# Optimization experiments

Hardware: AMD Instinct MI355X
Metric: run time of the kernel (lower is better)

The kernel has to match this reference:

```python
import jax, jax.numpy as jnp
import numpy as np

N_LAYERS = 2
D_MODEL = 1024
EXPAND = 2
D_INNER = EXPAND * D_MODEL   # 2048
D_STATE = 16
D_CONV = 4
DT_RANK = (D_MODEL + 15) // 16  # 64
BATCH = 2
SEQ = 1024


def setup_inputs() -> dict:
    key = jax.random.key(0)
    ks = jax.random.split(key, 8)
    x = jax.random.normal(ks[0], (BATCH, SEQ, D_MODEL), jnp.float32)
    in_proj_w = jax.random.normal(ks[1], (N_LAYERS, 2 * D_INNER, D_MODEL), jnp.float32) * 0.02
    conv_w = jax.random.normal(ks[2], (N_LAYERS, D_INNER, 1, D_CONV), jnp.float32) * 0.2
    conv_b = jnp.zeros((N_LAYERS, D_INNER), jnp.float32)
    x_proj_w = jax.random.normal(ks[3], (N_LAYERS, DT_RANK + 2 * D_STATE, D_INNER), jnp.float32) * 0.02
    dt_proj_w = jax.random.normal(ks[4], (N_LAYERS, D_INNER, DT_RANK), jnp.float32) * 0.1
    # softplus(b) ~ 0.01 -> realistic small dt init
    dt_proj_b = jnp.full((N_LAYERS, D_INNER), float(np.log(np.expm1(0.01))), jnp.float32)
    A_log = jnp.tile(jnp.log(jnp.arange(1, D_STATE + 1, dtype=jnp.float32))[None, None, :], (N_LAYERS, D_INNER, 1))
    D = jnp.ones((N_LAYERS, D_INNER), jnp.float32)
    out_proj_w = jax.random.normal(ks[5], (N_LAYERS, D_MODEL, D_INNER), jnp.float32) * 0.02
    return {
        'x': x, 'in_proj_w': in_proj_w, 'conv_w': conv_w, 'conv_b': conv_b,
        'x_proj_w': x_proj_w, 'dt_proj_w': dt_proj_w, 'dt_proj_b': dt_proj_b,
        'A_log': A_log, 'D': D, 'out_proj_w': out_proj_w,
    }


def _mamba_block(x, W_in, w_c, b_c, W_x, W_dt, b_dt, A_log, Dp, W_out):
    # x: (B, L, d_model)
    xz = jnp.einsum('bld,ed->ble', x, W_in)           # (B, L, 2*d_inner)
    xc, z = jnp.split(xz, 2, axis=-1)
    # causal depthwise conv1d over time
    xc = xc.transpose(0, 2, 1)                         # (B, d_inner, L)
    xc = jax.lax.conv_general_dilated(
        xc, w_c, window_strides=(1,), padding=[(D_CONV - 1, 0)],
        dimension_numbers=('NCH', 'OIH', 'NCH'), feature_group_count=D_INNER,
    ) + b_c[None, :, None]
    u = jax.nn.silu(xc).transpose(0, 2, 1)             # (B, L, d_inner)
    # input-dependent dt, B, C
    x_dbl = jnp.einsum('bld,ed->ble', u, W_x)          # (B, L, dt_rank+2N)
    dt, Bm, Cm = jnp.split(x_dbl, [DT_RANK, DT_RANK + D_STATE], axis=-1)
    delta = jax.nn.softplus(jnp.einsum('blr,dr->bld', dt, W_dt) + b_dt)  # (B, L, d_inner)
    A = -jnp.exp(A_log)                                 # (d_inner, N)
    dA = jnp.exp(jnp.einsum('bld,dn->bldn', delta, A))  # (B, L, d_inner, N)
    dBu = jnp.einsum('bld,bln,bld->bldn', delta, Bm, u) # (B, L, d_inner, N)

    def step(h, inp):
        dA_t, dBu_t, C_t = inp                          # (B,d,N), (B,d,N), (B,N)
        h = dA_t * h + dBu_t
        return h, jnp.einsum('bdn,bn->bd', h, C_t)

    h0 = jnp.zeros((x.shape[0], D_INNER, D_STATE), x.dtype)
    _, ys = jax.lax.scan(step, h0, (dA.transpose(1, 0, 2, 3), dBu.transpose(1, 0, 2, 3), Cm.transpose(1, 0, 2)))
    y = ys.transpose(1, 0, 2) + u * Dp                  # (B, L, d_inner)
    y = y * jax.nn.silu(z)
    return jnp.einsum('bld,od->blo', y, W_out)          # (B, L, d_model)


def _forward(x, in_proj_w, conv_w, conv_b, x_proj_w, dt_proj_w, dt_proj_b, A_log, D, out_proj_w):
    residual = x
    for i in range(N_LAYERS):
        x = _mamba_block(x, in_proj_w[i], conv_w[i], conv_b[i], x_proj_w[i],
                         dt_proj_w[i], dt_proj_b[i], A_log[i], D[i], out_proj_w[i])
    return x + residual


def reference(x, in_proj_w, conv_w, conv_b, x_proj_w, dt_proj_w, dt_proj_b, A_log, D, out_proj_w):
    return _forward(x, in_proj_w, conv_w, conv_b, x_proj_w, dt_proj_w, dt_proj_b, A_log, D, out_proj_w)
```

## Files before the change

kernel.cpp:

```cpp
#include <hip/hip_runtime.h>
#include <hip/hip_bf16.h>

#define NLAYERS 2
#define DMODEL 1024
#define DINNER 2048
#define DSTATE 16
#define DCONV 4
#define DTRANK 64
#define BATCH 2
#define SEQ 1024
#define TOK (BATCH * SEQ)

#define NCHUNK 32
#define CLEN (SEQ / NCHUNK)
#define KSX 16
#define KSO 4

typedef short bf16x8 __attribute__((ext_vector_type(8)));
typedef float f32x4 __attribute__((ext_vector_type(4)));
typedef unsigned short ushort8 __attribute__((ext_vector_type(8)));

__device__ __forceinline__ float softplusf(float x) {
    return (x > 20.f) ? x : log1pf(__expf(x));
}
__device__ __forceinline__ float siluf(float x) {
    return x / (1.f + __expf(-x));
}
__device__ __forceinline__ unsigned short f2bf(float f) {
    union { float f; unsigned int u; } v; v.f = f;
    const unsigned int r = (v.u + 0x7FFFu + ((v.u >> 16) & 1u)) >> 16;
    return (unsigned short)r;
}
__device__ __forceinline__ float bf2f(unsigned short s) {
    union { unsigned int u; float f; } v; v.u = ((unsigned int)s) << 16;
    return v.f;
}

__device__ __forceinline__ int swz_granule(int row, int kq) {
    return (row >> 1) * 8 + ((((row & 1) << 2) | kq) ^ ((row >> 1) & 7));
}

__device__ __forceinline__ void cvt8(const float* __restrict__ in,
                                     unsigned short* __restrict__ out, int i) {
    const float4 a = reinterpret_cast<const float4*>(in)[i * 2 + 0];
    const float4 b = reinterpret_cast<const float4*>(in)[i * 2 + 1];
    ushort4 o0, o1;
    o0.x = f2bf(a.x); o0.y = f2bf(a.y); o0.z = f2bf(a.z); o0.w = f2bf(a.w);
    o1.x = f2bf(b.x); o1.y = f2bf(b.y); o1.z = f2bf(b.z); o1.w = f2bf(b.w);
    reinterpret_cast<ushort4*>(out)[i * 2 + 0] = o0;
    reinterpret_cast<ushort4*>(out)[i * 2 + 1] = o1;
}

#define WI8 1048576
#define WO8 524288
#define WX8 49152
#define WD8 32768
#define AC8 262144
__global__ __launch_bounds__(256)
void cvt_all(const float* __restrict__ wi, const float* __restrict__ wo,
             const float* __restrict__ wx, const float* __restrict__ wd,
             const float* __restrict__ xin,
             unsigned short* __restrict__ wi_bf, unsigned short* __restrict__ wo_bf,
             unsigned short* __restrict__ wx_bf, unsigned short* __restrict__ wd_bf,
             unsigned short* __restrict__ act_bf) {
    int i = blockIdx.x * 256 + threadIdx.x;
    if (i < WI8) { cvt8(wi, wi_bf, i); return; }
    i -= WI8;
    if (i < WO8) { cvt8(wo, wo_bf, i); return; }
    i -= WO8;
    if (i < WX8) { cvt8(wx, wx_bf, i); return; }
    i -= WX8;
    if (i < WD8) { cvt8(wd, wd_bf, i); return; }
    i -= WD8;
    if (i < AC8) { cvt8(xin, act_bf, i); return; }
}

template <int EPI>
__global__ __launch_bounds__(256)
void gemm_bf16(const unsigned short* __restrict__ Ab, int lda,
               const unsigned short* __restrict__ Wb, int ldw,
               void* __restrict__ Cptr, int ldc, int kLen, int Nw,
               size_t cSlice, const float* __restrict__ bias) {
    __shared__ unsigned short As[2][128 * 32];
    __shared__ unsigned short Bs[2][128 * 32];
    const int tid = threadIdx.x;
    const int wave = tid >> 6, lane = tid & 63;
    const int wr = wave >> 1, wc = wave & 1;
    const int m0 = blockIdx.y * 128, n0 = blockIdx.x * 128;
    const int kbeg = blockIdx.z * kLen;
    const int r = lane & 15, kq = lane >> 4;
    const int nt = kLen >> 5;

    const int ch0 = tid, ch1 = 256 + tid;
    const int g0 = ch0 >> 3, p0 = ch0 & 7, lp0 = p0 ^ (g0 & 7);
    const int srow0 = (g0 << 1) | (lp0 >> 2), skq0 = lp0 & 3;
    const int g1 = ch1 >> 3, p1 = ch1 & 7, lp1 = p1 ^ (g1 & 7);
    const int srow1 = (g1 << 1) | (lp1 >> 2), skq1 = lp1 & 3;
    const int wrow0 = min(n0 + srow0, Nw - 1);
    const int wrow1 = min(n0 + srow1, Nw - 1);

    auto stage = [&](int buf, int kt) {
        __builtin_amdgcn_global_load_lds(
            (const __attribute__((address_space(1))) void*)
                &Ab[(size_t)(m0 + srow0) * lda + kt + skq0 * 8],
            (__attribute__((address_space(3))) void*)&As[buf][ch0 * 8], 16, 0, 0);
        __builtin_amdgcn_global_load_lds(
            (const __attribute__((address_space(1))) void*)
                &Wb[(size_t)wrow0 * ldw + kt + skq0 * 8],
            (__attribute__((address_space(3))) void*)&Bs[buf][ch0 * 8], 16, 0, 0);
        __builtin_amdgcn_global_load_lds(
            (const __attribute__((address_space(1))) void*)
                &Ab[(size_t)(m0 + srow1) * lda + kt + skq1 * 8],
            (__attribute__((address_space(3))) void*)&As[buf][ch1 * 8], 16, 0, 0);
        __builtin_amdgcn_global_load_lds(
            (const __attribute__((address_space(1))) void*)
                &Wb[(size_t)wrow1 * ldw + kt + skq1 * 8],
            (__attribute__((address_space(3))) void*)&Bs[buf][ch1 * 8], 16, 0, 0);
    };

    int aoff[4], boff[4];
#pragma unroll
    for (int f = 0; f < 4; ++f) {
        aoff[f] = swz_granule(wr * 64 + f * 16 + r, kq) * 8;
        boff[f] = swz_granule(wc * 64 + f * 16 + r, kq) * 8;
    }

    f32x4 acc[4][4] = {};
    stage(0, kbeg);
    for (int t = 0; t < nt; ++t) {
        const int cur = t & 1;
        if (t + 1 < nt) {
            stage(cur ^ 1, kbeg + (t + 1) * 32);
            asm volatile("s_waitcnt vmcnt(4)" ::: "memory");
        } else {
            asm volatile("s_waitcnt vmcnt(0)" ::: "memory");
        }
        __builtin_amdgcn_s_barrier();
        __builtin_amdgcn_sched_barrier(0);
        bf16x8 a[4], b[4];
#pragma unroll
        for (int f = 0; f < 4; ++f) {
            a[f] = *reinterpret_cast<const bf16x8*>(&As[cur][aoff[f]]);
            b[f] = *reinterpret_cast<const bf16x8*>(&Bs[cur][boff[f]]);
        }
#pragma unroll
        for (int fi = 0; fi < 4; ++fi)
#pragma unroll
            for (int fj = 0; fj < 4; ++fj)
                acc[fi][fj] = __builtin_amdgcn_mfma_f32_16x16x32_bf16(
                    a[fi], b[fj], acc[fi][fj], 0, 0, 0);
        __builtin_amdgcn_sched_barrier(0);
        asm volatile("s_waitcnt lgkmcnt(0)" ::: "memory");
        __builtin_amdgcn_s_barrier();
    }

    const int cr = lane >> 4, cc = lane & 15;
#pragma unroll
    for (int fi = 0; fi < 4; ++fi)
#pragma unroll
        for (int fj = 0; fj < 4; ++fj)
#pragma unroll
            for (int p = 0; p < 4; ++p) {
                const int m = m0 + wr * 64 + fi * 16 + cr * 4 + p;
                const int n = n0 + wc * 64 + fj * 16 + cc;
                const float v = acc[fi][fj][p];
                if (EPI == 0) {
                    if (n < Nw)
                        ((float*)Cptr)[(size_t)blockIdx.z * cSlice +
                                       (size_t)m * ldc + n] = v;
                } else if (EPI == 3) {
                    ((unsigned short*)Cptr)[(size_t)blockIdx.z * cSlice +
                                            (size_t)m * ldc + n] = f2bf(v);
                } else if (EPI == 4) {
                    ((unsigned short*)Cptr)[(size_t)m * ldc + n] =
                        f2bf(softplusf(v + bias[n]));
                } else {
                    if (n < Nw)
                        ((unsigned short*)Cptr)[(size_t)blockIdx.z * cSlice +
                                                (size_t)m * ldc + n] = f2bf(v);
                }
            }
}

__global__ __launch_bounds__(256)
void conv_silu8(const unsigned short* __restrict__ xz_bf,
                const float* __restrict__ cw,
                const float* __restrict__ cb,
                unsigned short* __restrict__ u_bf) {
    const int gid = blockIdx.x * 256 + threadIdx.x;
    const int d8 = gid & 255;
    const int t = gid >> 8;
    const int l = t & (SEQ - 1);
    const int d0 = d8 * 8;

    float cwv[8][4];
#pragma unroll
    for (int j = 0; j < 8; ++j) {
        const float4 c = *reinterpret_cast<const float4*>(&cw[(d0 + j) * DCONV]);
        cwv[j][0] = c.x; cwv[j][1] = c.y; cwv[j][2] = c.z; cwv[j][3] = c.w;
    }
    float acc[8];
    {
        const float4 b0 = *reinterpret_cast<const float4*>(&cb[d0]);
        const float4 b1 = *reinterpret_cast<const float4*>(&cb[d0 + 4]);
        acc[0] = b0.x; acc[1] = b0.y; acc[2] = b0.z; acc[3] = b0.w;
        acc[4] = b1.x; acc[5] = b1.y; acc[6] = b1.z; acc[7] = b1.w;
    }
#pragma unroll
    for (int k = 0; k < DCONV; ++k) {
        const int li = l - (DCONV - 1) + k;
        if (li >= 0) {
            const ushort8 v = *reinterpret_cast<const ushort8*>(
                &xz_bf[(size_t)(t - (DCONV - 1) + k) * 4096 + d0]);
#pragma unroll
            for (int j = 0; j < 8; ++j)
                acc[j] = fmaf(cwv[j][k], bf2f(v[j]), acc[j]);
        }
    }
    ushort8 o;
#pragma unroll
    for (int j = 0; j < 8; ++j) o[j] = f2bf(siluf(acc[j]));
    *reinterpret_cast<ushort8*>(&u_bf[(size_t)t * DINNER + d0]) = o;
}

__global__ __launch_bounds__(256)
void reduce_x(const unsigned short* __restrict__ part, float* __restrict__ xdbl,
              unsigned short* __restrict__ dt_bf) {
    const int i = blockIdx.x * 256 + threadIdx.x;
    if (i >= TOK * 96) return;
    float s = 0.f;
#pragma unroll
    for (int k = 0; k < KSX; ++k) s += bf2f(part[(size_t)k * (TOK * 96) + i]);
    xdbl[i] = s;
    const int t = i / 96, c = i - t * 96;
    if (c < DTRANK) dt_bf[t * DTRANK + c] = f2bf(s);
}

template <int MODE>
__global__ __launch_bounds__(256)
void reduce_out(const unsigned short* __restrict__ part,
                const float* __restrict__ resid, void* __restrict__ outp) {
    const int i = blockIdx.x * 256 + threadIdx.x;
    if (i >= TOK * DMODEL / 4) return;
    float s[4] = {0.f, 0.f, 0.f, 0.f};
#pragma unroll
    for (int k = 0; k < KSO; ++k) {
        const ushort4 p = reinterpret_cast<const ushort4*>(
            &part[(size_t)k * (TOK * DMODEL)])[i];
        s[0] += bf2f(p.x); s[1] += bf2f(p.y); s[2] += bf2f(p.z); s[3] += bf2f(p.w);
    }
    if (MODE == 0) {
        ushort4 o;
        o.x = f2bf(s[0]); o.y = f2bf(s[1]); o.z = f2bf(s[2]); o.w = f2bf(s[3]);
        reinterpret_cast<ushort4*>(outp)[i] = o;
    } else {
        const float4 rr = reinterpret_cast<const float4*>(resid)[i];
        float4 o;
        o.x = s[0] + rr.x; o.y = s[1] + rr.y; o.z = s[2] + rr.z; o.w = s[3] + rr.w;
        reinterpret_cast<float4*>(outp)[i] = o;
    }
}

__device__ __forceinline__ void load_b16(const float* __restrict__ p, float* B) {
    const float4* bp = reinterpret_cast<const float4*>(p);
    const float4 b0 = bp[0], b1 = bp[1], b2 = bp[2], b3 = bp[3];
    B[0] = b0.x; B[1] = b0.y; B[2] = b0.z; B[3] = b0.w;
    B[4] = b1.x; B[5] = b1.y; B[6] = b1.z; B[7] = b1.w;
    B[8] = b2.x; B[9] = b2.y; B[10] = b2.z; B[11] = b2.w;
    B[12] = b3.x; B[13] = b3.y; B[14] = b3.z; B[15] = b3.w;
}
__device__ __forceinline__ void load_bf16x16(const unsigned short* __restrict__ p,
                                             float* B) {
    const ushort8 v0 = *reinterpret_cast<const ushort8*>(p);
    const ushort8 v1 = *reinterpret_cast<const ushort8*>(p + 8);
#pragma unroll
    for (int j = 0; j < 8; ++j) { B[j] = bf2f(v0[j]); B[8 + j] = bf2f(v1[j]); }
}
__device__ __forceinline__ void store_bf16x16(unsigned short* __restrict__ p,
                                              const float* B) {
    ushort8 v0, v1;
#pragma unroll
    for (int j = 0; j < 8; ++j) { v0[j] = f2bf(B[j]); v1[j] = f2bf(B[8 + j]); }
    *reinterpret_cast<ushort8*>(p) = v0;
    *reinterpret_cast<ushort8*>(p + 8) = v1;
}

__global__ __launch_bounds__(256)
void scan_partial(const unsigned short* __restrict__ delta_bf,
                  const unsigned short* __restrict__ u_bf,
                  const float* __restrict__ xdbl,
                  const float* __restrict__ A_log,
                  unsigned short* __restrict__ hbuf,
                  unsigned short* __restrict__ Pbuf) {
    const int b = blockIdx.y / NCHUNK;
    const int c = blockIdx.y % NCHUNK;
    const int d = blockIdx.x * 256 + threadIdx.x;
    const int t0 = b * SEQ + c * CLEN;

    float A_dn[16];
    load_b16(&A_log[d * DSTATE], A_dn);
#pragma unroll
    for (int n = 0; n < 16; ++n) A_dn[n] = -__expf(A_dn[n]);

    float h[16];
#pragma unroll
    for (int n = 0; n < 16; ++n) h[n] = 0.f;
    float sdlt = 0.f;

    float dltA, uvA, BA[16];
    float dltB, uvB, BB[16];
    dltA = bf2f(delta_bf[(size_t)t0 * DINNER + d]);
    uvA = bf2f(u_bf[(size_t)t0 * DINNER + d]);
    load_b16(&xdbl[(size_t)t0 * 96 + DTRANK], BA);

#define PSTEP(dlt_, uv_, Bc_)                              \
    {                                                      \
        const float du = (dlt_) * (uv_);                   \
        sdlt += (dlt_);                                    \
        _Pragma("unroll")                                  \
        for (int n = 0; n < 16; ++n) {                     \
            const float dA = __expf((dlt_) * A_dn[n]);     \
            h[n] = fmaf(dA, h[n], du * Bc_[n]);            \
        }                                                  \
    }

    for (int l = 0; l < CLEN; l += 2) {
        const int t = t0 + l;
        dltB = bf2f(delta_bf[(size_t)(t + 1) * DINNER + d]);
        uvB = bf2f(u_bf[(size_t)(t + 1) * DINNER + d]);
        load_b16(&xdbl[(size_t)(t + 1) * 96 + DTRANK], BB);
        PSTEP(dltA, uvA, BA);
        if (l + 2 < CLEN) {
            dltA = bf2f(delta_bf[(size_t)(t + 2) * DINNER + d]);
            uvA = bf2f(u_bf[(size_t)(t + 2) * DINNER + d]);
            load_b16(&xdbl[(size_t)(t + 2) * 96 + DTRANK], BA);
        }
        PSTEP(dltB, uvB, BB);
    }
#undef PSTEP

    float P[16];
#pragma unroll
    for (int n = 0; n < 16; ++n) P[n] = __expf(sdlt * A_dn[n]);

    const size_t base = ((size_t)(b * NCHUNK + c) * DINNER + d) * DSTATE;
    store_bf16x16(&hbuf[base], h);
    store_bf16x16(&Pbuf[base], P);
}

__global__ __launch_bounds__(256)
void scan_combine(unsigned short* __restrict__ hbuf,
                  const unsigned short* __restrict__ Pbuf) {
    const int gid = blockIdx.x * 256 + threadIdx.x;
    const int b = gid / (DINNER * DSTATE);
    const int dn = gid - b * (DINNER * DSTATE);
    const size_t base = (size_t)b * NCHUNK * DINNER * DSTATE + dn;
    float hv[NCHUNK], Pv[NCHUNK];
#pragma unroll
    for (int c = 0; c < NCHUNK; ++c) {
        const size_t idx = base + (size_t)c * (DINNER * DSTATE);
        hv[c] = bf2f(hbuf[idx]);
        Pv[c] = bf2f(Pbuf[idx]);
    }
    float hi = 0.f;
#pragma unroll
    for (int c = 0; c < NCHUNK; ++c) {
        const size_t idx = base + (size_t)c * (DINNER * DSTATE);
        hbuf[idx] = f2bf(hi);
        hi = fmaf(Pv[c], hi, hv[c]);
    }
}

__global__ __launch_bounds__(256)
void scan_final(const unsigned short* __restrict__ delta_bf,
                const unsigned short* __restrict__ u_bf,
                const float* __restrict__ xdbl,
                const unsigned short* __restrict__ xz_bf,
                const float* __restrict__ A_log,
                const float* __restrict__ Dp,
                const unsigned short* __restrict__ hbuf,
                unsigned short* __restrict__ yout) {
    const int b = blockIdx.y / NCHUNK;
    const int c = blockIdx.y % NCHUNK;
    const int d = blockIdx.x * 256 + threadIdx.x;
    const int t0 = b * SEQ + c * CLEN;

    float A_dn[16];
    load_b16(&A_log[d * DSTATE], A_dn);
#pragma unroll
    for (int n = 0; n < 16; ++n) A_dn[n] = -__expf(A_dn[n]);
    const float Dd = Dp[d];

    float h[16];
    load_bf16x16(&hbuf[((size_t)(b * NCHUNK + c) * DINNER + d) * DSTATE], h);

    float dltA, uvA, BA[16], CA[16];
    float dltB, uvB, BB[16], CB[16];
    dltA = bf2f(delta_bf[(size_t)t0 * DINNER + d]);
    uvA = bf2f(u_bf[(size_t)t0 * DINNER + d]);
    load_b16(&xdbl[(size_t)t0 * 96 + DTRANK], BA);
    load_b16(&xdbl[(size_t)t0 * 96 + DTRANK + DSTATE], CA);

#define FSTEP(t_, dlt_, uv_, Bc_, Cc_)                          \
    {                                                           \
        const float du = (dlt_) * (uv_);                        \
        _Pragma("unroll")                                       \
        for (int n = 0; n < 16; ++n) {                          \
            const float dA = __expf((dlt_) * A_dn[n]);          \
            h[n] = fmaf(dA, h[n], du * Bc_[n]);                 \
        }                                                       \
        float s0 = 0.f, s1 = 0.f, s2 = 0.f, s3 = 0.f;           \
        _Pragma("unroll")                                       \
        for (int q = 0; q < 4; ++q) {                           \
            s0 = fmaf(h[q*4+0], Cc_[q*4+0], s0);                \
            s1 = fmaf(h[q*4+1], Cc_[q*4+1], s1);                \
            s2 = fmaf(h[q*4+2], Cc_[q*4+2], s2);                \
            s3 = fmaf(h[q*4+3], Cc_[q*4+3], s3);                \
        }                                                       \
        const float zv = bf2f(xz_bf[(size_t)(t_) * 4096 + 2048 + d]); \
        const float y = (s0 + s1) + (s2 + s3) + (uv_) * Dd;     \
        yout[(size_t)(t_) * DINNER + d] = f2bf(y * siluf(zv));  \
    }

    for (int l = 0; l < CLEN; l += 2) {
        const int t = t0 + l;
        dltB = bf2f(delta_bf[(size_t)(t + 1) * DINNER + d]);
        uvB = bf2f(u_bf[(size_t)(t + 1) * DINNER + d]);
        load_b16(&xdbl[(size_t)(t + 1) * 96 + DTRANK], BB);
        load_b16(&xdbl[(size_t)(t + 1) * 96 + DTRANK + DSTATE], CB);
        FSTEP(t, dltA, uvA, BA, CA);
        if (l + 2 < CLEN) {
            dltA = bf2f(delta_bf[(size_t)(t + 2) * DINNER + d]);
            uvA = bf2f(u_bf[(size_t)(t + 2) * DINNER + d]);
            load_b16(&xdbl[(size_t)(t + 2) * 96 + DTRANK], BA);
            load_b16(&xdbl[(size_t)(t + 2) * 96 + DTRANK + DSTATE], CA);
        }
        FSTEP(t + 1, dltB, uvB, BB, CB);
    }
#undef FSTEP
}

extern "C" void kernel_launch(void* const* d_in, const int* in_sizes, int n_in,
                              void* d_out, int out_size, void* d_ws, size_t ws_size,
                              hipStream_t stream) {
    const float* x          = (const float*)d_in[0];
    const float* in_proj_w  = (const float*)d_in[1];
    const float* conv_w     = (const float*)d_in[2];
    const float* conv_b     = (const float*)d_in[3];
    const float* x_proj_w   = (const float*)d_in[4];
    const float* dt_proj_w  = (const float*)d_in[5];
    const float* dt_proj_b  = (const float*)d_in[6];
    const float* A_log      = (const float*)d_in[7];
    const float* Dp         = (const float*)d_in[8];
    const float* out_proj_w = (const float*)d_in[9];
    float* out = (float*)d_out;

    float* ws = (float*)d_ws;
    float* xdbl  = ws;
    unsigned short* us = (unsigned short*)(xdbl + 196608);
    unsigned short* xpart  = us;
    unsigned short* hbuf   = xpart + 3145728;
    unsigned short* Pbuf   = hbuf + 2097152;
    unsigned short* opart  = Pbuf + 2097152;
    unsigned short* wi_bf  = opart + 8388608;
    unsigned short* wo_bf  = wi_bf + 8388608;
    unsigned short* wx_bf  = wo_bf + 4194304;
    unsigned short* wd_bf  = wx_bf + 393216;
    unsigned short* xz_bf  = wd_bf + 262144;
    unsigned short* u_bf   = xz_bf + 8388608;
    unsigned short* dlt_bf = u_bf  + 4194304;
    unsigned short* act_bf = dlt_bf + 4194304;
    unsigned short* y_bf   = act_bf + 2097152;
    unsigned short* dt_bf  = y_bf  + 4194304;

    cvt_all<<<(WI8 + WO8 + WX8 + WD8 + AC8 + 255) / 256, 256, 0, stream>>>(
        in_proj_w, out_proj_w, x_proj_w, dt_proj_w, x,
        wi_bf, wo_bf, wx_bf, wd_bf, act_bf);

    for (int layer = 0; layer < NLAYERS; ++layer) {
        const unsigned short* Wi = wi_bf + (size_t)layer * (2 * DINNER) * DMODEL;
        const unsigned short* Wo = wo_bf + (size_t)layer * DMODEL * DINNER;
        const unsigned short* Wx = wx_bf + (size_t)layer * 96 * DINNER;
        const unsigned short* Wd = wd_bf + (size_t)layer * DINNER * DTRANK;
        const float* cw = conv_w    + (size_t)layer * DINNER * DCONV;
        const float* cb = conv_b    + (size_t)layer * DINNER;
        const float* bd = dt_proj_b + (size_t)layer * DINNER;
        const float* Al = A_log     + (size_t)layer * DINNER * DSTATE;
        const float* Dl = Dp        + (size_t)layer * DINNER;

        {
            dim3 grid(4096 / 128, TOK / 128, 1);
            gemm_bf16<3><<<grid, 256, 0, stream>>>(act_bf, DMODEL, Wi, DMODEL,
                                                   xz_bf, 2 * DINNER, DMODEL,
                                                   2 * DINNER, 0, nullptr);
        }
        conv_silu8<<<(TOK * 256) / 256, 256, 0, stream>>>(xz_bf, cw, cb, u_bf);
        {
            dim3 grid(1, TOK / 128, KSX);
            gemm_bf16<5><<<grid, 256, 0, stream>>>(u_bf, DINNER, Wx, DINNER,
                                                   xpart, 96, DINNER / KSX, 96,
                                                   (size_t)TOK * 96, nullptr);
            reduce_x<<<(TOK * 96 + 255) / 256, 256, 0, stream>>>(xpart, xdbl, dt_bf);
        }
        {
            dim3 grid(DINNER / 128, TOK / 128, 1);
            gemm_bf16<4><<<grid, 256, 0, stream>>>(dt_bf, DTRANK, Wd, DTRANK,
                                                   dlt_bf, DINNER, DTRANK, DINNER,
                                                   0, bd);
        }
        {
            dim3 gridA(DINNER / 256, BATCH * NCHUNK);
            scan_partial<<<gridA, 256, 0, stream>>>(dlt_bf, u_bf, xdbl, Al,
                                                    hbuf, Pbuf);
            scan_combine<<<(BATCH * DINNER * DSTATE) / 256, 256, 0, stream>>>(hbuf, Pbuf);
            scan_final<<<gridA, 256, 0, stream>>>(dlt_bf, u_bf, xdbl, xz_bf,
                                                  Al, Dl, hbuf, y_bf);
        }
        {
            dim3 grid(DMODEL / 128, TOK / 128, KSO);
            gemm_bf16<3><<<grid, 256, 0, stream>>>(y_bf, DINNER, Wo, DINNER,
                                                   opart, DMODEL, DINNER / KSO,
                                                   DMODEL, (size_t)TOK * DMODEL,
                                                   nullptr);
            const int nred = TOK * DMODEL / 4;
            if (layer == NLAYERS - 1) {
                reduce_out<1><<<(nred + 255) / 256, 256, 0, stream>>>(opart, x, out);
            } else {
                reduce_out<0><<<(nred + 255) / 256, 256, 0, stream>>>(opart, nullptr,
                                                                      act_bf);
            }
        }
    }
}
```

Baseline: 320.5 us.

## Fold scan combine into final scan, pack B/C as bf16, remap GEMM tile order

Removes the scan_combine kernel: each scan_final block now recomputes its chunk-initial state by iterating over all preceding chunks' partial states and decay products, which adds redundant work that grows with the chunk index. B and C are stored as a compact bf16 array of 32 values per token instead of fp32 inside the 96-wide xdbl buffer, which halves the bytes read per step in the scans but loses precision on B and C. GEMM workgroup IDs are remapped in interleaved groups of eight, apparently to spread neighbouring tiles across XCDs or improve cache locality. The unused fp32 epilogue is dropped.

New measurement: 340.6 us. +6.3%, slower.

```diff
diff --git a/kernel.cpp b/kernel.cpp
--- a/kernel.cpp
+++ b/kernel.cpp
@@ -86,7 +86,14 @@
     const int tid = threadIdx.x;
     const int wave = tid >> 6, lane = tid & 63;
     const int wr = wave >> 1, wc = wave & 1;
-    const int m0 = blockIdx.y * 128, n0 = blockIdx.x * 128;
+
+    const int nwg = gridDim.x * gridDim.y;
+    const int id0 = blockIdx.y * gridDim.x + blockIdx.x;
+    const int cpx = nwg >> 3;
+    const int id = (id0 & 7) * cpx + (id0 >> 3);
+    const int bx = id % gridDim.x, by = id / gridDim.x;
+
+    const int m0 = by * 128, n0 = bx * 128;
     const int kbeg = blockIdx.z * kLen;
     const int r = lane & 15, kq = lane >> 4;
     const int nt = kLen >> 5;
@@ -164,11 +171,7 @@
                 const int m = m0 + wr * 64 + fi * 16 + cr * 4 + p;
                 const int n = n0 + wc * 64 + fj * 16 + cc;
                 const float v = acc[fi][fj][p];
-                if (EPI == 0) {
-                    if (n < Nw)
-                        ((float*)Cptr)[(size_t)blockIdx.z * cSlice +
-                                       (size_t)m * ldc + n] = v;
-                } else if (EPI == 3) {
+                if (EPI == 3) {
                     ((unsigned short*)Cptr)[(size_t)blockIdx.z * cSlice +
                                             (size_t)m * ldc + n] = f2bf(v);
                 } else if (EPI == 4) {
@@ -224,16 +227,17 @@
 }
 
 __global__ __launch_bounds__(256)
-void reduce_x(const unsigned short* __restrict__ part, float* __restrict__ xdbl,
+void reduce_x(const unsigned short* __restrict__ part,
+              unsigned short* __restrict__ bc_bf,
               unsigned short* __restrict__ dt_bf) {
     const int i = blockIdx.x * 256 + threadIdx.x;
     if (i >= TOK * 96) return;
     float s = 0.f;
 #pragma unroll
     for (int k = 0; k < KSX; ++k) s += bf2f(part[(size_t)k * (TOK * 96) + i]);
-    xdbl[i] = s;
     const int t = i / 96, c = i - t * 96;
     if (c < DTRANK) dt_bf[t * DTRANK + c] = f2bf(s);
+    else            bc_bf[t * 32 + (c - DTRANK)] = f2bf(s);
 }
 
 template <int MODE>
@@ -288,7 +292,7 @@
 __global__ __launch_bounds__(256)
 void scan_partial(const unsigned short* __restrict__ delta_bf,
                   const unsigned short* __restrict__ u_bf,
-                  const float* __restrict__ xdbl,
+                  const unsigned short* __restrict__ bc_bf,
                   const float* __restrict__ A_log,
                   unsigned short* __restrict__ hbuf,
                   unsigned short* __restrict__ Pbuf) {
@@ -311,7 +315,7 @@
     float dltB, uvB, BB[16];
     dltA = bf2f(delta_bf[(size_t)t0 * DINNER + d]);
     uvA = bf2f(u_bf[(size_t)t0 * DINNER + d]);
-    load_b16(&xdbl[(size_t)t0 * 96 + DTRANK], BA);
+    load_bf16x16(&bc_bf[(size_t)t0 * 32], BA);
 
 #define PSTEP(dlt_, uv_, Bc_)                              \
     {                                                      \
@@ -328,12 +332,12 @@
         const int t = t0 + l;
         dltB = bf2f(delta_bf[(size_t)(t + 1) * DINNER + d]);
         uvB = bf2f(u_bf[(size_t)(t + 1) * DINNER + d]);
-        load_b16(&xdbl[(size_t)(t + 1) * 96 + DTRANK], BB);
+        load_bf16x16(&bc_bf[(size_t)(t + 1) * 32], BB);
         PSTEP(dltA, uvA, BA);
         if (l + 2 < CLEN) {
             dltA = bf2f(delta_bf[(size_t)(t + 2) * DINNER + d]);
             uvA = bf2f(u_bf[(size_t)(t + 2) * DINNER + d]);
-            load_b16(&xdbl[(size_t)(t + 2) * 96 + DTRANK], BA);
+            load_bf16x16(&bc_bf[(size_t)(t + 2) * 32], BA);
         }
         PSTEP(dltB, uvB, BB);
     }
@@ -349,36 +353,14 @@
 }
 
 __global__ __launch_bounds__(256)
-void scan_combine(unsigned short* __restrict__ hbuf,
-                  const unsigned short* __restrict__ Pbuf) {
-    const int gid = blockIdx.x * 256 + threadIdx.x;
-    const int b = gid / (DINNER * DSTATE);
-    const int dn = gid - b * (DINNER * DSTATE);
-    const size_t base = (size_t)b * NCHUNK * DINNER * DSTATE + dn;
-    float hv[NCHUNK], Pv[NCHUNK];
-#pragma unroll
-    for (int c = 0; c < NCHUNK; ++c) {
-        const size_t idx = base + (size_t)c * (DINNER * DSTATE);
-        hv[c] = bf2f(hbuf[idx]);
-        Pv[c] = bf2f(Pbuf[idx]);
-    }
-    float hi = 0.f;
-#pragma unroll
-    for (int c = 0; c < NCHUNK; ++c) {
-        const size_t idx = base + (size_t)c * (DINNER * DSTATE);
-        hbuf[idx] = f2bf(hi);
-        hi = fmaf(Pv[c], hi, hv[c]);
-    }
-}
-
-__global__ __launch_bounds__(256)
 void scan_final(const unsigned short* __restrict__ delta_bf,
                 const unsigned short* __restrict__ u_bf,
-                const float* __restrict__ xdbl,
+                const unsigned short* __restrict__ bc_bf,
                 const unsigned short* __restrict__ xz_bf,
                 const float* __restrict__ A_log,
                 const float* __restrict__ Dp,
                 const unsigned short* __restrict__ hbuf,
+                const unsigned short* __restrict__ Pbuf,
                 unsigned short* __restrict__ yout) {
     const int b = blockIdx.y / NCHUNK;
     const int c = blockIdx.y % NCHUNK;
@@ -392,14 +374,23 @@
     const float Dd = Dp[d];
 
     float h[16];
-    load_bf16x16(&hbuf[((size_t)(b * NCHUNK + c) * DINNER + d) * DSTATE], h);
+#pragma unroll
+    for (int n = 0; n < 16; ++n) h[n] = 0.f;
+    for (int cc = 0; cc < c; ++cc) {
+        const size_t base = ((size_t)(b * NCHUNK + cc) * DINNER + d) * DSTATE;
+        float hl[16], Pc[16];
+        load_bf16x16(&hbuf[base], hl);
+        load_bf16x16(&Pbuf[base], Pc);
+#pragma unroll
+        for (int n = 0; n < 16; ++n) h[n] = fmaf(Pc[n], h[n], hl[n]);
+    }
 
     float dltA, uvA, BA[16], CA[16];
     float dltB, uvB, BB[16], CB[16];
     dltA = bf2f(delta_bf[(size_t)t0 * DINNER + d]);
     uvA = bf2f(u_bf[(size_t)t0 * DINNER + d]);
-    load_b16(&xdbl[(size_t)t0 * 96 + DTRANK], BA);
-    load_b16(&xdbl[(size_t)t0 * 96 + DTRANK + DSTATE], CA);
+    load_bf16x16(&bc_bf[(size_t)t0 * 32], BA);
+    load_bf16x16(&bc_bf[(size_t)t0 * 32 + 16], CA);
 
 #define FSTEP(t_, dlt_, uv_, Bc_, Cc_)                          \
     {                                                           \
@@ -426,14 +417,14 @@
         const int t = t0 + l;
         dltB = bf2f(delta_bf[(size_t)(t + 1) * DINNER + d]);
         uvB = bf2f(u_bf[(size_t)(t + 1) * DINNER + d]);
-        load_b16(&xdbl[(size_t)(t + 1) * 96 + DTRANK], BB);
-        load_b16(&xdbl[(size_t)(t + 1) * 96 + DTRANK + DSTATE], CB);
+        load_bf16x16(&bc_bf[(size_t)(t + 1) * 32], BB);
+        load_bf16x16(&bc_bf[(size_t)(t + 1) * 32 + 16], CB);
         FSTEP(t, dltA, uvA, BA, CA);
         if (l + 2 < CLEN) {
             dltA = bf2f(delta_bf[(size_t)(t + 2) * DINNER + d]);
             uvA = bf2f(u_bf[(size_t)(t + 2) * DINNER + d]);
-            load_b16(&xdbl[(size_t)(t + 2) * 96 + DTRANK], BA);
-            load_b16(&xdbl[(size_t)(t + 2) * 96 + DTRANK + DSTATE], CA);
+            load_bf16x16(&bc_bf[(size_t)(t + 2) * 32], BA);
+            load_bf16x16(&bc_bf[(size_t)(t + 2) * 32 + 16], CA);
         }
         FSTEP(t + 1, dltB, uvB, BB, CB);
     }
@@ -455,11 +446,10 @@
     const float* out_proj_w = (const float*)d_in[9];
     float* out = (float*)d_out;
 
-    float* ws = (float*)d_ws;
-    float* xdbl  = ws;
-    unsigned short* us = (unsigned short*)(xdbl + 196608);
+    unsigned short* us = (unsigned short*)d_ws;
     unsigned short* xpart  = us;
-    unsigned short* hbuf   = xpart + 3145728;
+    unsigned short* bc_bf  = xpart + 3145728;
+    unsigned short* hbuf   = bc_bf + 65536;
     unsigned short* Pbuf   = hbuf + 2097152;
     unsigned short* opart  = Pbuf + 2097152;
     unsigned short* wi_bf  = opart + 8388608;
@@ -500,7 +490,8 @@
             gemm_bf16<5><<<grid, 256, 0, stream>>>(u_bf, DINNER, Wx, DINNER,
                                                    xpart, 96, DINNER / KSX, 96,
                                                    (size_t)TOK * 96, nullptr);
-            reduce_x<<<(TOK * 96 + 255) / 256, 256, 0, stream>>>(xpart, xdbl, dt_bf);
+            reduce_x<<<(TOK * 96 + 255) / 256, 256, 0, stream>>>(xpart, bc_bf,
+                                                                 dt_bf);
         }
         {
             dim3 grid(DINNER / 128, TOK / 128, 1);
@@ -510,11 +501,10 @@
         }
         {
             dim3 gridA(DINNER / 256, BATCH * NCHUNK);
-            scan_partial<<<gridA, 256, 0, stream>>>(dlt_bf, u_bf, xdbl, Al,
+            scan_partial<<<gridA, 256, 0, stream>>>(dlt_bf, u_bf, bc_bf, Al,
                                                     hbuf, Pbuf);
-            scan_combine<<<(BATCH * DINNER * DSTATE) / 256, 256, 0, stream>>>(hbuf, Pbuf);
-            scan_final<<<gridA, 256, 0, stream>>>(dlt_bf, u_bf, xdbl, xz_bf,
-                                                  Al, Dl, hbuf, y_bf);
+            scan_final<<<gridA, 256, 0, stream>>>(dlt_bf, u_bf, bc_bf, xz_bf,
+                                                  Al, Dl, hbuf, Pbuf, y_bf);
         }
         {
             dim3 grid(DMODEL / 128, TOK / 128, KSO);
```

## Fuse chunked scan passes into one cooperative kernel with grid syncs

Applied to the files above, without the earlier changes.

Merges the three scan kernels (per-chunk partial scan, cross-chunk combine, final output scan) into one cooperative launch that separates the phases with grid-wide syncs. The aim is to remove two kernel launches and their launch gaps per layer. The grid is 8x64 = 512 blocks of 256 threads, and every block must be co-resident for the cooperative launch to work. Register pressure from holding the combine arrays may also lower occupancy. The now-unused EPI==0 GEMM epilogue is also removed.

Result: slower. 805.6 us (+151.4%).

```diff
diff --git a/kernel.cpp b/kernel.cpp
--- a/kernel.cpp
+++ b/kernel.cpp
@@ -1,5 +1,8 @@
 #include <hip/hip_runtime.h>
 #include <hip/hip_bf16.h>
+#include <hip/hip_cooperative_groups.h>
+
+namespace cg = cooperative_groups;
 
 #define NLAYERS 2
 #define DMODEL 1024
@@ -164,11 +167,7 @@
                 const int m = m0 + wr * 64 + fi * 16 + cr * 4 + p;
                 const int n = n0 + wc * 64 + fj * 16 + cc;
                 const float v = acc[fi][fj][p];
-                if (EPI == 0) {
-                    if (n < Nw)
-                        ((float*)Cptr)[(size_t)blockIdx.z * cSlice +
-                                       (size_t)m * ldc + n] = v;
-                } else if (EPI == 3) {
+                if (EPI == 3) {
                     ((unsigned short*)Cptr)[(size_t)blockIdx.z * cSlice +
                                             (size_t)m * ldc + n] = f2bf(v);
                 } else if (EPI == 4) {
@@ -286,100 +285,16 @@
 }
 
 __global__ __launch_bounds__(256)
-void scan_partial(const unsigned short* __restrict__ delta_bf,
-                  const unsigned short* __restrict__ u_bf,
-                  const float* __restrict__ xdbl,
-                  const float* __restrict__ A_log,
-                  unsigned short* __restrict__ hbuf,
-                  unsigned short* __restrict__ Pbuf) {
-    const int b = blockIdx.y / NCHUNK;
-    const int c = blockIdx.y % NCHUNK;
-    const int d = blockIdx.x * 256 + threadIdx.x;
-    const int t0 = b * SEQ + c * CLEN;
-
-    float A_dn[16];
-    load_b16(&A_log[d * DSTATE], A_dn);
-#pragma unroll
-    for (int n = 0; n < 16; ++n) A_dn[n] = -__expf(A_dn[n]);
-
-    float h[16];
-#pragma unroll
-    for (int n = 0; n < 16; ++n) h[n] = 0.f;
-    float sdlt = 0.f;
-
-    float dltA, uvA, BA[16];
-    float dltB, uvB, BB[16];
-    dltA = bf2f(delta_bf[(size_t)t0 * DINNER + d]);
-    uvA = bf2f(u_bf[(size_t)t0 * DINNER + d]);
-    load_b16(&xdbl[(size_t)t0 * 96 + DTRANK], BA);
-
-#define PSTEP(dlt_, uv_, Bc_)                              \
-    {                                                      \
-        const float du = (dlt_) * (uv_);                   \
-        sdlt += (dlt_);                                    \
-        _Pragma("unroll")                                  \
-        for (int n = 0; n < 16; ++n) {                     \
-            const float dA = __expf((dlt_) * A_dn[n]);     \
-            h[n] = fmaf(dA, h[n], du * Bc_[n]);            \
-        }                                                  \
-    }
-
-    for (int l = 0; l < CLEN; l += 2) {
-        const int t = t0 + l;
-        dltB = bf2f(delta_bf[(size_t)(t + 1) * DINNER + d]);
-        uvB = bf2f(u_bf[(size_t)(t + 1) * DINNER + d]);
-        load_b16(&xdbl[(size_t)(t + 1) * 96 + DTRANK], BB);
-        PSTEP(dltA, uvA, BA);
-        if (l + 2 < CLEN) {
-            dltA = bf2f(delta_bf[(size_t)(t + 2) * DINNER + d]);
-            uvA = bf2f(u_bf[(size_t)(t + 2) * DINNER + d]);
-            load_b16(&xdbl[(size_t)(t + 2) * 96 + DTRANK], BA);
-        }
-        PSTEP(dltB, uvB, BB);
-    }
-#undef PSTEP
-
-    float P[16];
-#pragma unroll
-    for (int n = 0; n < 16; ++n) P[n] = __expf(sdlt * A_dn[n]);
-
-    const size_t base = ((size_t)(b * NCHUNK + c) * DINNER + d) * DSTATE;
-    store_bf16x16(&hbuf[base], h);
-    store_bf16x16(&Pbuf[base], P);
-}
-
-__global__ __launch_bounds__(256)
-void scan_combine(unsigned short* __restrict__ hbuf,
-                  const unsigned short* __restrict__ Pbuf) {
-    const int gid = blockIdx.x * 256 + threadIdx.x;
-    const int b = gid / (DINNER * DSTATE);
-    const int dn = gid - b * (DINNER * DSTATE);
-    const size_t base = (size_t)b * NCHUNK * DINNER * DSTATE + dn;
-    float hv[NCHUNK], Pv[NCHUNK];
-#pragma unroll
-    for (int c = 0; c < NCHUNK; ++c) {
-        const size_t idx = base + (size_t)c * (DINNER * DSTATE);
-        hv[c] = bf2f(hbuf[idx]);
-        Pv[c] = bf2f(Pbuf[idx]);
-    }
-    float hi = 0.f;
-#pragma unroll
-    for (int c = 0; c < NCHUNK; ++c) {
-        const size_t idx = base + (size_t)c * (DINNER * DSTATE);
-        hbuf[idx] = f2bf(hi);
-        hi = fmaf(Pv[c], hi, hv[c]);
-    }
-}
-
-__global__ __launch_bounds__(256)
-void scan_final(const unsigned short* __restrict__ delta_bf,
+void scan_fused(const unsigned short* __restrict__ delta_bf,
                 const unsigned short* __restrict__ u_bf,
                 const float* __restrict__ xdbl,
                 const unsigned short* __restrict__ xz_bf,
                 const float* __restrict__ A_log,
                 const float* __restrict__ Dp,
-                const unsigned short* __restrict__ hbuf,
+                unsigned short* __restrict__ hbuf,
+                unsigned short* __restrict__ Pbuf,
                 unsigned short* __restrict__ yout) {
+    cg::grid_group grid = cg::this_grid();
     const int b = blockIdx.y / NCHUNK;
     const int c = blockIdx.y % NCHUNK;
     const int d = blockIdx.x * 256 + threadIdx.x;
@@ -389,55 +304,133 @@
     load_b16(&A_log[d * DSTATE], A_dn);
 #pragma unroll
     for (int n = 0; n < 16; ++n) A_dn[n] = -__expf(A_dn[n]);
-    const float Dd = Dp[d];
-
-    float h[16];
-    load_bf16x16(&hbuf[((size_t)(b * NCHUNK + c) * DINNER + d) * DSTATE], h);
-
-    float dltA, uvA, BA[16], CA[16];
-    float dltB, uvB, BB[16], CB[16];
-    dltA = bf2f(delta_bf[(size_t)t0 * DINNER + d]);
-    uvA = bf2f(u_bf[(size_t)t0 * DINNER + d]);
-    load_b16(&xdbl[(size_t)t0 * 96 + DTRANK], BA);
-    load_b16(&xdbl[(size_t)t0 * 96 + DTRANK + DSTATE], CA);
+
+    {
+        float h[16];
+#pragma unroll
+        for (int n = 0; n < 16; ++n) h[n] = 0.f;
+        float sdlt = 0.f;
+
+        float dltA, uvA, BA[16];
+        float dltB, uvB, BB[16];
+        dltA = bf2f(delta_bf[(size_t)t0 * DINNER + d]);
+        uvA = bf2f(u_bf[(size_t)t0 * DINNER + d]);
+        load_b16(&xdbl[(size_t)t0 * 96 + DTRANK], BA);
+
+#define PSTEP(dlt_, uv_, Bc_)                              \
+        {                                                  \
+            const float du = (dlt_) * (uv_);               \
+            sdlt += (dlt_);                                \
+            _Pragma("unroll")                              \
+            for (int n = 0; n < 16; ++n) {                 \
+                const float dA = __expf((dlt_) * A_dn[n]); \
+                h[n] = fmaf(dA, h[n], du * Bc_[n]);        \
+            }                                              \
+        }
+
+        for (int l = 0; l < CLEN; l += 2) {
+            const int t = t0 + l;
+            dltB = bf2f(delta_bf[(size_t)(t + 1) * DINNER + d]);
+            uvB = bf2f(u_bf[(size_t)(t + 1) * DINNER + d]);
+            load_b16(&xdbl[(size_t)(t + 1) * 96 + DTRANK], BB);
+            PSTEP(dltA, uvA, BA);
+            if (l + 2 < CLEN) {
+                dltA = bf2f(delta_bf[(size_t)(t + 2) * DINNER + d]);
+                uvA = bf2f(u_bf[(size_t)(t + 2) * DINNER + d]);
+                load_b16(&xdbl[(size_t)(t + 2) * 96 + DTRANK], BA);
+            }
+            PSTEP(dltB, uvB, BB);
+        }
+#undef PSTEP
+
+        float P[16];
+#pragma unroll
+        for (int n = 0; n < 16; ++n) P[n] = __expf(sdlt * A_dn[n]);
+
+        const size_t base = ((size_t)(b * NCHUNK + c) * DINNER + d) * DSTATE;
+        store_bf16x16(&hbuf[base], h);
+        store_bf16x16(&Pbuf[base], P);
+    }
+
+    __threadfence();
+    grid.sync();
+
+    {
+        const int flat = (blockIdx.y * gridDim.x + blockIdx.x) * 256 + threadIdx.x;
+        if (flat < BATCH * DINNER * DSTATE) {
+            const int b2 = flat / (DINNER * DSTATE);
+            const int dn = flat - b2 * (DINNER * DSTATE);
+            const size_t base = (size_t)b2 * NCHUNK * DINNER * DSTATE + dn;
+            float hv[NCHUNK], Pv[NCHUNK];
+#pragma unroll
+            for (int cc = 0; cc < NCHUNK; ++cc) {
+                const size_t idx = base + (size_t)cc * (DINNER * DSTATE);
+                hv[cc] = bf2f(hbuf[idx]);
+                Pv[cc] = bf2f(Pbuf[idx]);
+            }
+            float hi = 0.f;
+#pragma unroll
+            for (int cc = 0; cc < NCHUNK; ++cc) {
+                const size_t idx = base + (size_t)cc * (DINNER * DSTATE);
+                hbuf[idx] = f2bf(hi);
+                hi = fmaf(Pv[cc], hi, hv[cc]);
+            }
+        }
+    }
+
+    __threadfence();
+    grid.sync();
+
+    {
+        const float Dd = Dp[d];
+        float h[16];
+        load_bf16x16(&hbuf[((size_t)(b * NCHUNK + c) * DINNER + d) * DSTATE], h);
+
+        float dltA, uvA, BA[16], CA[16];
+        float dltB, uvB, BB[16], CB[16];
+        dltA = bf2f(delta_bf[(size_t)t0 * DINNER + d]);
+        uvA = bf2f(u_bf[(size_t)t0 * DINNER + d]);
+        load_b16(&xdbl[(size_t)t0 * 96 + DTRANK], BA);
+        load_b16(&xdbl[(size_t)t0 * 96 + DTRANK + DSTATE], CA);
 
 #define FSTEP(t_, dlt_, uv_, Bc_, Cc_)                          \
-    {                                                           \
-        const float du = (dlt_) * (uv_);                        \
-        _Pragma("unroll")                                       \
-        for (int n = 0; n < 16; ++n) {                          \
-            const float dA = __expf((dlt_) * A_dn[n]);          \
-            h[n] = fmaf(dA, h[n], du * Bc_[n]);                 \
-        }                                                       \
-        float s0 = 0.f, s1 = 0.f, s2 = 0.f, s3 = 0.f;           \
-        _Pragma("unroll")                                       \
-        for (int q = 0; q < 4; ++q) {                           \
-            s0 = fmaf(h[q*4+0], Cc_[q*4+0], s0);                \
-            s1 = fmaf(h[q*4+1], Cc_[q*4+1], s1);                \
-            s2 = fmaf(h[q*4+2], Cc_[q*4+2], s2);                \
-            s3 = fmaf(h[q*4+3], Cc_[q*4+3], s3);                \
-        }                                                       \
-        const float zv = bf2f(xz_bf[(size_t)(t_) * 4096 + 2048 + d]); \
-        const float y = (s0 + s1) + (s2 + s3) + (uv_) * Dd;     \
-        yout[(size_t)(t_) * DINNER + d] = f2bf(y * siluf(zv));  \
-    }
-
-    for (int l = 0; l < CLEN; l += 2) {
-        const int t = t0 + l;
-        dltB = bf2f(delta_bf[(size_t)(t + 1) * DINNER + d]);
-        uvB = bf2f(u_bf[(size_t)(t + 1) * DINNER + d]);
-        load_b16(&xdbl[(size_t)(t + 1) * 96 + DTRANK], BB);
-        load_b16(&xdbl[(size_t)(t + 1) * 96 + DTRANK + DSTATE], CB);
-        FSTEP(t, dltA, uvA, BA, CA);
-        if (l + 2 < CLEN) {
-            dltA = bf2f(delta_bf[(size_t)(t + 2) * DINNER + d]);
-            uvA = bf2f(u_bf[(size_t)(t + 2) * DINNER + d]);
-            load_b16(&xdbl[(size_t)(t + 2) * 96 + DTRANK], BA);
-            load_b16(&xdbl[(size_t)(t + 2) * 96 + DTRANK + DSTATE], CA);
-        }
-        FSTEP(t + 1, dltB, uvB, BB, CB);
-    }
+        {                                                       \
+            const float du = (dlt_) * (uv_);                    \
+            _Pragma("unroll")                                   \
+            for (int n = 0; n < 16; ++n) {                      \
+                const float dA = __expf((dlt_) * A_dn[n]);      \
+                h[n] = fmaf(dA, h[n], du * Bc_[n]);             \
+            }                                                   \
+            float s0 = 0.f, s1 = 0.f, s2 = 0.f, s3 = 0.f;       \
+            _Pragma("unroll")                                   \
+            for (int q = 0; q < 4; ++q) {                       \
+                s0 = fmaf(h[q*4+0], Cc_[q*4+0], s0);            \
+                s1 = fmaf(h[q*4+1], Cc_[q*4+1], s1);            \
+                s2 = fmaf(h[q*4+2], Cc_[q*4+2], s2);            \
+                s3 = fmaf(h[q*4+3], Cc_[q*4+3], s3);            \
+            }                                                   \
+            const float zv = bf2f(xz_bf[(size_t)(t_) * 4096 + 2048 + d]); \
+            const float y = (s0 + s1) + (s2 + s3) + (uv_) * Dd; \
+            yout[(size_t)(t_) * DINNER + d] = f2bf(y * siluf(zv)); \
+        }
+
+        for (int l = 0; l < CLEN; l += 2) {
+            const int t = t0 + l;
+            dltB = bf2f(delta_bf[(size_t)(t + 1) * DINNER + d]);
+            uvB = bf2f(u_bf[(size_t)(t + 1) * DINNER + d]);
+            load_b16(&xdbl[(size_t)(t + 1) * 96 + DTRANK], BB);
+            load_b16(&xdbl[(size_t)(t + 1) * 96 + DTRANK + DSTATE], CB);
+            FSTEP(t, dltA, uvA, BA, CA);
+            if (l + 2 < CLEN) {
+                dltA = bf2f(delta_bf[(size_t)(t + 2) * DINNER + d]);
+                uvA = bf2f(u_bf[(size_t)(t + 2) * DINNER + d]);
+                load_b16(&xdbl[(size_t)(t + 2) * 96 + DTRANK], BA);
+                load_b16(&xdbl[(size_t)(t + 2) * 96 + DTRANK + DSTATE], CA);
+            }
+            FSTEP(t + 1, dltB, uvB, BB, CB);
+        }
 #undef FSTEP
+    }
 }
 
 extern "C" void kernel_launch(void* const* d_in, const int* in_sizes, int n_in,
@@ -509,12 +502,12 @@
                                                    0, bd);
         }
         {
-            dim3 gridA(DINNER / 256, BATCH * NCHUNK);
-            scan_partial<<<gridA, 256, 0, stream>>>(dlt_bf, u_bf, xdbl, Al,
-                                                    hbuf, Pbuf);
-            scan_combine<<<(BATCH * DINNER * DSTATE) / 256, 256, 0, stream>>>(hbuf, Pbuf);
-            scan_final<<<gridA, 256, 0, stream>>>(dlt_bf, u_bf, xdbl, xz_bf,
-                                                  Al, Dl, hbuf, y_bf);
+            void* args[] = {(void*)&dlt_bf, (void*)&u_bf, (void*)&xdbl,
+                            (void*)&xz_bf, (void*)&Al, (void*)&Dl,
+                            (void*)&hbuf, (void*)&Pbuf, (void*)&y_bf};
+            hipLaunchCooperativeKernel((void*)scan_fused,
+                                       dim3(DINNER / 256, BATCH * NCHUNK),
+                                       dim3(256), args, 0, stream);
         }
         {
             dim3 grid(DMODEL / 128, TOK / 128, KSO);
```
